# Kernel optimization log

Hardware: AMD Instinct MI355X
Metric: run time of the kernel (lower is better)

## Reference

```python
import jax, jax.numpy as jnp
import numpy as np

W_NBITS = 8
A_NBITS = 8


def _fake_quant_weight_per_channel(w, nbits):
    # symmetric per-output-channel (row) fake quantization
    qmax = float(2 ** (nbits - 1) - 1)
    scale = jnp.max(jnp.abs(w), axis=1, keepdims=True) / qmax  # [out, 1]
    scale = jnp.maximum(scale, 1e-8)
    return jnp.clip(jnp.round(w / scale), -qmax - 1.0, qmax) * scale


def _fake_quant_act_per_group(x, group_size, nbits):
    # dynamic symmetric per-group fake quantization along the feature dim
    qmax = float(2 ** (nbits - 1) - 1)
    tokens, feat = x.shape
    xg = x.reshape(tokens, feat // group_size, group_size)
    scale = jnp.max(jnp.abs(xg), axis=-1, keepdims=True) / qmax  # [T, G, 1]
    scale = jnp.maximum(scale, 1e-8)
    xq = jnp.clip(jnp.round(xg / scale), -qmax - 1.0, qmax) * scale
    return xq.reshape(tokens, feat)


def setup_inputs() -> dict:
    key = jax.random.key(0)
    k1, k2, k3 = jax.random.split(key, 3)
    tokens, in_f, out_f = 8192, 4096, 4096
    x = jax.random.normal(k1, (tokens, in_f), dtype=jnp.float32)
    weight = jax.random.normal(k2, (out_f, in_f), dtype=jnp.float32) * 0.02
    bias = jax.random.normal(k3, (out_f,), dtype=jnp.float32) * 0.02
    return {"x": x, "weight": weight, "bias": bias, "group_size": 128}


def reference(x, weight, bias, group_size):
    w_q = _fake_quant_weight_per_channel(weight, W_NBITS)
    x_q = _fake_quant_act_per_group(x, group_size, A_NBITS)
    # F.linear: x @ w.T + b
    return jnp.einsum("tc,oc->to", x_q, w_q) + bias
```

## Files before the change

kernel.cpp:

```cpp
#include <hip/hip_runtime.h>
#include <stdint.h>


typedef __attribute__((ext_vector_type(4))) int   i32x4;
typedef __attribute__((ext_vector_type(4))) float f32x4;

static __device__ __forceinline__ void load_lds16(const void* g, void* l) {
    __builtin_amdgcn_global_load_lds(
        (const __attribute__((address_space(1))) void*)g,
        (__attribute__((address_space(3))) void*)l, 16, 0, 0);
}

static __device__ __forceinline__ int8_t q8m(float v, float inv) {
    float q = rintf(v * inv);
    q = fminf(fmaxf(q, -128.0f), 127.0f);
    return (int8_t)(int)q;
}

__global__ __launch_bounds__(256) void quant_act_kernel(
        const float* __restrict__ x, int8_t* __restrict__ xq,
        float* __restrict__ sxT, int M) {
    const int row = blockIdx.x, t = threadIdx.x;
    const float* xr = x + (size_t)row * 4096;
    float4 v[4];
#pragma unroll
    for (int i = 0; i < 4; i++)
        v[i] = *(const float4*)(xr + t * 16 + i * 4);
    float m = 0.0f;
#pragma unroll
    for (int i = 0; i < 4; i++)
        m = fmaxf(m, fmaxf(fmaxf(fabsf(v[i].x), fabsf(v[i].y)),
                           fmaxf(fabsf(v[i].z), fabsf(v[i].w))));
    m = fmaxf(m, __shfl_xor(m, 1));
    m = fmaxf(m, __shfl_xor(m, 2));
    m = fmaxf(m, __shfl_xor(m, 4));
    const float scale = fmaxf(m / 127.0f, 1e-8f);
    const float inv = 1.0f / scale;
    union { int8_t b[16]; i32x4 w; } o;
#pragma unroll
    for (int i = 0; i < 4; i++) {
        o.b[i * 4 + 0] = q8m(v[i].x, inv);
        o.b[i * 4 + 1] = q8m(v[i].y, inv);
        o.b[i * 4 + 2] = q8m(v[i].z, inv);
        o.b[i * 4 + 3] = q8m(v[i].w, inv);
    }
    *(i32x4*)(xq + (size_t)row * 4096 + t * 16) = o.w;
    if ((t & 7) == 0)
        sxT[(size_t)(t >> 3) * M + row] = scale;
}

__global__ __launch_bounds__(256) void quant_wgt_kernel(
        const float* __restrict__ w, int8_t* __restrict__ wq,
        float* __restrict__ sw) {
    const int row = blockIdx.x, t = threadIdx.x;
    const float* wr = w + (size_t)row * 4096;
    float4 v[4];
#pragma unroll
    for (int i = 0; i < 4; i++)
        v[i] = *(const float4*)(wr + t * 16 + i * 4);
    float m = 0.0f;
#pragma unroll
    for (int i = 0; i < 4; i++)
        m = fmaxf(m, fmaxf(fmaxf(fabsf(v[i].x), fabsf(v[i].y)),
                           fmaxf(fabsf(v[i].z), fabsf(v[i].w))));
#pragma unroll
    for (int off = 1; off < 64; off <<= 1)
        m = fmaxf(m, __shfl_xor(m, off));
    __shared__ float wm[4];
    if ((t & 63) == 0) wm[t >> 6] = m;
    __syncthreads();
    m = fmaxf(fmaxf(wm[0], wm[1]), fmaxf(wm[2], wm[3]));
    const float scale = fmaxf(m / 127.0f, 1e-8f);
    if (t == 0) sw[row] = scale;
    const float inv = 1.0f / scale;
    union { int8_t b[16]; i32x4 w4; } o;
#pragma unroll
    for (int i = 0; i < 4; i++) {
        o.b[i * 4 + 0] = q8m(v[i].x, inv);
        o.b[i * 4 + 1] = q8m(v[i].y, inv);
        o.b[i * 4 + 2] = q8m(v[i].z, inv);
        o.b[i * 4 + 3] = q8m(v[i].w, inv);
    }
    *(i32x4*)(wq + (size_t)row * 4096 + t * 16) = o.w4;
}

#define QUAD(mh, nh)                                                         \
    _Pragma("unroll")                                                        \
    for (int mi2 = 0; mi2 < 4; ++mi2) {                                      \
        _Pragma("unroll")                                                    \
        for (int nj = 0; nj < 2; ++nj) {                                     \
            const int ni = (nh) * 2 + nj;                                    \
            i32x4 t = __builtin_amdgcn_mfma_i32_16x16x64_i8(                 \
                a[mi2][0], b[ni][0], (i32x4){0, 0, 0, 0}, 0, 0, 0);          \
            t = __builtin_amdgcn_mfma_i32_16x16x64_i8(                       \
                a[mi2][1], b[ni][1], t, 0, 0, 0);                            \
            _Pragma("unroll")                                                \
            for (int r = 0; r < 4; ++r)                                      \
                acc[(mh) * 4 + mi2][ni][r] += (float)t[r] * sxv[mi2][r];     \
        }                                                                    \
    }

__global__ __launch_bounds__(512, 2) void gemm_i8_kernel(
        const int8_t* __restrict__ A, const int8_t* __restrict__ B,
        const float* __restrict__ sxT, const float* __restrict__ sw,
        const float* __restrict__ bias, float* __restrict__ C,
        int M, int N, int K) {
    __shared__ __align__(16) int8_t As[2][256 * 128];
    __shared__ __align__(16) int8_t Bs[2][256 * 128];
    const int tid = threadIdx.x;
    const int wave = tid >> 6, lane = tid & 63;

    const int nwg = gridDim.x, nN = N >> 8;
    const int wg = ((int)blockIdx.x & 7) * (nwg >> 3) + ((int)blockIdx.x >> 3);
    const int bm = (wg / nN) << 8, bn = (wg % nN) << 8;

    const int wm = (wave >> 2) << 7, wn = (wave & 3) << 6;
    const int fr = lane & 15, q = lane >> 4, r7 = lane & 7;

    const int srow = wave * 8 + (lane >> 3);
    const int scol = ((lane & 7) ^ ((lane >> 3) & 7)) << 4;
    const size_t sK = (size_t)K;
    const int8_t* Ag = A + (size_t)(bm + srow) * sK + scol;
    const int8_t* Bg = B + (size_t)(bn + srow) * sK + scol;
    const int sldsw = wave * 8 * 128;

    f32x4 acc[8][4];
#pragma unroll
    for (int i = 0; i < 8; i++)
#pragma unroll
        for (int jn = 0; jn < 4; jn++) acc[i][jn] = (f32x4){0.f, 0.f, 0.f, 0.f};

    const int abase = (wm + fr) * 128;
    const int bbase = (wn + fr) * 128;
    const int c0 = (q ^ r7) << 4, c1 = ((4 + q) ^ r7) << 4;
    const float* sxw = sxT + bm + wm + q * 4;

    const int NT = K >> 7;

    load_lds16(Bg,             &Bs[0][sldsw]);
    load_lds16(Bg +  64 * sK,  &Bs[0][ 64 * 128 + sldsw]);
    load_lds16(Bg + 128 * sK,  &Bs[0][128 * 128 + sldsw]);
    load_lds16(Bg + 192 * sK,  &Bs[0][192 * 128 + sldsw]);
    load_lds16(Ag,             &As[0][sldsw]);
    load_lds16(Ag + 128 * sK,  &As[0][128 * 128 + sldsw]);
    load_lds16(Ag +  64 * sK,  &As[0][ 64 * 128 + sldsw]);
    load_lds16(Ag + 192 * sK,  &As[0][192 * 128 + sldsw]);
    asm volatile("s_waitcnt vmcnt(2)" ::: "memory");
    __builtin_amdgcn_s_barrier();

    for (int j = 0; j < NT; ++j) {
        const int cur = j & 1, nxt = cur ^ 1;
        const size_t kn = (size_t)((j + 1 < NT) ? j + 1 : j) << 7;
        const int8_t* Ac = As[cur];
        const int8_t* Bc = Bs[cur];
        const float* sxg = sxw + (size_t)j * M;

        i32x4 a[4][2], b[4][2];
        f32x4 sxv[4];

#pragma unroll
        for (int i = 0; i < 4; ++i) {
            a[i][0] = *(const i32x4*)(Ac + abase + i * 2048 + c0);
            a[i][1] = *(const i32x4*)(Ac + abase + i * 2048 + c1);
            b[i][0] = *(const i32x4*)(Bc + bbase + i * 2048 + c0);
            b[i][1] = *(const i32x4*)(Bc + bbase + i * 2048 + c1);
        }
#pragma unroll
        for (int i = 0; i < 4; ++i)
            sxv[i] = *(const f32x4*)(sxg + i * 16);
        load_lds16(Bg + kn,            &Bs[nxt][sldsw]);
        load_lds16(Bg + kn + 64 * sK,  &Bs[nxt][64 * 128 + sldsw]);
        __builtin_amdgcn_s_barrier();
        asm volatile("s_waitcnt lgkmcnt(0)" ::: "memory");
        __builtin_amdgcn_sched_barrier(0);
        __builtin_amdgcn_s_setprio(1);
        QUAD(0, 0)
        __builtin_amdgcn_s_setprio(0);
        __builtin_amdgcn_s_barrier();

        load_lds16(Bg + kn + 128 * sK, &Bs[nxt][128 * 128 + sldsw]);
        load_lds16(Bg + kn + 192 * sK, &Bs[nxt][192 * 128 + sldsw]);
        __builtin_amdgcn_s_barrier();
        __builtin_amdgcn_sched_barrier(0);
        __builtin_amdgcn_s_setprio(1);
        QUAD(0, 1)
        __builtin_amdgcn_s_setprio(0);
        asm volatile("s_waitcnt vmcnt(4)" ::: "memory");
        __builtin_amdgcn_s_barrier();

#pragma unroll
        for (int i = 0; i < 4; ++i) {
            a[i][0] = *(const i32x4*)(Ac + abase + 64 * 128 + i * 2048 + c0);
            a[i][1] = *(const i32x4*)(Ac + abase + 64 * 128 + i * 2048 + c1);
        }
#pragma unroll
        for (int i = 0; i < 4; ++i)
            sxv[i] = *(const f32x4*)(sxg + 64 + i * 16);
        load_lds16(Ag + kn,            &As[nxt][sldsw]);
        load_lds16(Ag + kn + 128 * sK, &As[nxt][128 * 128 + sldsw]);
        __builtin_amdgcn_s_barrier();
        asm volatile("s_waitcnt lgkmcnt(0)" ::: "memory");
        __builtin_amdgcn_sched_barrier(0);
        __builtin_amdgcn_s_setprio(1);
        QUAD(1, 0)
        __builtin_amdgcn_s_setprio(0);
        __builtin_amdgcn_s_barrier();

        load_lds16(Ag + kn + 64 * sK,  &As[nxt][64 * 128 + sldsw]);
        load_lds16(Ag + kn + 192 * sK, &As[nxt][192 * 128 + sldsw]);
        __builtin_amdgcn_s_barrier();
        __builtin_amdgcn_sched_barrier(0);
        __builtin_amdgcn_s_setprio(1);
        QUAD(1, 1)
        __builtin_amdgcn_s_setprio(0);
        asm volatile("s_waitcnt vmcnt(2)" ::: "memory");
        __builtin_amdgcn_s_barrier();
    }
    asm volatile("s_waitcnt vmcnt(0)" ::: "memory");

    const int or0 = bm + wm + q * 4;
    const int oc0 = bn + wn + fr;
    float swv[4], bv[4];
#pragma unroll
    for (int ni = 0; ni < 4; ni++) {
        swv[ni] = sw[oc0 + ni * 16];
        bv[ni] = bias[oc0 + ni * 16];
    }
#pragma unroll
    for (int mi = 0; mi < 8; mi++)
#pragma unroll
        for (int ni = 0; ni < 4; ni++)
#pragma unroll
            for (int r = 0; r < 4; r++)
                C[(size_t)(or0 + mi * 16 + r) * N + (oc0 + ni * 16)] =
                    acc[mi][ni][r] * swv[ni] + bv[ni];
}

extern "C" void kernel_launch(void* const* d_in, const int* in_sizes, int n_in,
                              void* d_out, int out_size, void* d_ws, size_t ws_size,
                              hipStream_t stream) {
    const float* x    = (const float*)d_in[0];
    const float* w    = (const float*)d_in[1];
    const float* bias = (const float*)d_in[2];

    const int out_f  = in_sizes[2];
    const int in_f   = in_sizes[1] / out_f;
    const int tokens = in_sizes[0] / in_f;
    const int G = in_f / 128;

    int8_t* xq  = (int8_t*)d_ws;
    int8_t* wq  = xq + (size_t)tokens * in_f;
    float*  sxT = (float*)(wq + (size_t)out_f * in_f);
    float*  sw  = sxT + (size_t)G * tokens;
    float*  out = (float*)d_out;

    quant_act_kernel<<<tokens, 256, 0, stream>>>(x, xq, sxT, tokens);
    quant_wgt_kernel<<<out_f, 256, 0, stream>>>(w, wq, sw);

    const int nwg = (tokens / 256) * (out_f / 256);
    gemm_i8_kernel<<<nwg, 512, 0, stream>>>(xq, wq, sxT, sw, bias, out,
                                            tokens, out_f, in_f);
}
```

Measured before the change: 475.4 us.

## Prefetch activation scales a tile ahead and reload B fragments per half-phase

Per-group activation scales for the next K tile are now fetched from global memory at the end of each iteration into an 8-entry register array, instead of being loaded synchronously right before each compute phase. This hides the scale load latency behind the LDS-to-global pipeline, and the vmcnt waits are adjusted to match. B fragments are now loaded two at a time just before each compute phase, which reduces register pressure but adds extra LDS reads and waits. MFMAs are grouped four at a time per B column to lengthen independent chains before the scale-and-accumulate step.

```diff
diff --git a/kernel.cpp b/kernel.cpp
--- a/kernel.cpp
+++ b/kernel.cpp
@@ -84,20 +84,23 @@
     *(i32x4*)(wq + (size_t)row * 4096 + t * 16) = o.w4;
 }
 
-#define QUAD(mh, nh)                                                         \
+#define COMPUTE(mh, nh)                                                      \
     _Pragma("unroll")                                                        \
-    for (int mi2 = 0; mi2 < 4; ++mi2) {                                      \
+    for (int g = 0; g < 2; ++g) {                                            \
+        i32x4 it[4];                                                         \
         _Pragma("unroll")                                                    \
-        for (int nj = 0; nj < 2; ++nj) {                                     \
-            const int ni = (nh) * 2 + nj;                                    \
-            i32x4 t = __builtin_amdgcn_mfma_i32_16x16x64_i8(                 \
-                a[mi2][0], b[ni][0], (i32x4){0, 0, 0, 0}, 0, 0, 0);          \
-            t = __builtin_amdgcn_mfma_i32_16x16x64_i8(                       \
-                a[mi2][1], b[ni][1], t, 0, 0, 0);                            \
+        for (int mi = 0; mi < 4; ++mi) {                                     \
+            it[mi] = __builtin_amdgcn_mfma_i32_16x16x64_i8(                  \
+                a[mi][0], b[g][0], (i32x4){0, 0, 0, 0}, 0, 0, 0);            \
+            it[mi] = __builtin_amdgcn_mfma_i32_16x16x64_i8(                  \
+                a[mi][1], b[g][1], it[mi], 0, 0, 0);                         \
+        }                                                                    \
+        _Pragma("unroll")                                                    \
+        for (int mi = 0; mi < 4; ++mi)                                       \
             _Pragma("unroll")                                                \
             for (int r = 0; r < 4; ++r)                                      \
-                acc[(mh) * 4 + mi2][ni][r] += (float)t[r] * sxv[mi2][r];     \
-        }                                                                    \
+                acc[(mh) * 4 + mi][(nh) * 2 + g][r] +=                       \
+                    (float)it[mi][r] * sxn[(mh) * 4 + mi][r];                \
     }
 
 __global__ __launch_bounds__(512, 2) void gemm_i8_kernel(
@@ -133,7 +136,7 @@
     const int abase = (wm + fr) * 128;
     const int bbase = (wn + fr) * 128;
     const int c0 = (q ^ r7) << 4, c1 = ((4 + q) ^ r7) << 4;
-    const float* sxw = sxT + bm + wm + q * 4;
+    const float* sxp = sxT + bm + wm + q * 4;
 
     const int NT = K >> 7;
 
@@ -145,7 +148,11 @@
     load_lds16(Ag + 128 * sK,  &As[0][128 * 128 + sldsw]);
     load_lds16(Ag +  64 * sK,  &As[0][ 64 * 128 + sldsw]);
     load_lds16(Ag + 192 * sK,  &As[0][192 * 128 + sldsw]);
-    asm volatile("s_waitcnt vmcnt(2)" ::: "memory");
+    f32x4 sxn[8];
+#pragma unroll
+    for (int i = 0; i < 8; ++i)
+        sxn[i] = *(const f32x4*)(sxp + (i >> 2) * 64 + (i & 3) * 16);
+    asm volatile("s_waitcnt vmcnt(10)" ::: "memory");
     __builtin_amdgcn_s_barrier();
 
     for (int j = 0; j < NT; ++j) {
@@ -153,37 +160,41 @@
         const size_t kn = (size_t)((j + 1 < NT) ? j + 1 : j) << 7;
         const int8_t* Ac = As[cur];
         const int8_t* Bc = Bs[cur];
-        const float* sxg = sxw + (size_t)j * M;
-
-        i32x4 a[4][2], b[4][2];
-        f32x4 sxv[4];
+
+        i32x4 a[4][2], b[2][2];
 
 #pragma unroll
         for (int i = 0; i < 4; ++i) {
             a[i][0] = *(const i32x4*)(Ac + abase + i * 2048 + c0);
             a[i][1] = *(const i32x4*)(Ac + abase + i * 2048 + c1);
+        }
+#pragma unroll
+        for (int i = 0; i < 2; ++i) {
             b[i][0] = *(const i32x4*)(Bc + bbase + i * 2048 + c0);
             b[i][1] = *(const i32x4*)(Bc + bbase + i * 2048 + c1);
         }
-#pragma unroll
-        for (int i = 0; i < 4; ++i)
-            sxv[i] = *(const f32x4*)(sxg + i * 16);
         load_lds16(Bg + kn,            &Bs[nxt][sldsw]);
         load_lds16(Bg + kn + 64 * sK,  &Bs[nxt][64 * 128 + sldsw]);
         __builtin_amdgcn_s_barrier();
         asm volatile("s_waitcnt lgkmcnt(0)" ::: "memory");
         __builtin_amdgcn_sched_barrier(0);
         __builtin_amdgcn_s_setprio(1);
-        QUAD(0, 0)
-        __builtin_amdgcn_s_setprio(0);
-        __builtin_amdgcn_s_barrier();
-
+        COMPUTE(0, 0)
+        __builtin_amdgcn_s_setprio(0);
+        __builtin_amdgcn_s_barrier();
+
+#pragma unroll
+        for (int i = 0; i < 2; ++i) {
+            b[i][0] = *(const i32x4*)(Bc + bbase + (2 + i) * 2048 + c0);
+            b[i][1] = *(const i32x4*)(Bc + bbase + (2 + i) * 2048 + c1);
+        }
         load_lds16(Bg + kn + 128 * sK, &Bs[nxt][128 * 128 + sldsw]);
         load_lds16(Bg + kn + 192 * sK, &Bs[nxt][192 * 128 + sldsw]);
         __builtin_amdgcn_s_barrier();
-        __builtin_amdgcn_sched_barrier(0);
-        __builtin_amdgcn_s_setprio(1);
-        QUAD(0, 1)
+        asm volatile("s_waitcnt lgkmcnt(0)" ::: "memory");
+        __builtin_amdgcn_sched_barrier(0);
+        __builtin_amdgcn_s_setprio(1);
+        COMPUTE(0, 1)
         __builtin_amdgcn_s_setprio(0);
         asm volatile("s_waitcnt vmcnt(4)" ::: "memory");
         __builtin_amdgcn_s_barrier();
@@ -194,26 +205,40 @@
             a[i][1] = *(const i32x4*)(Ac + abase + 64 * 128 + i * 2048 + c1);
         }
 #pragma unroll
-        for (int i = 0; i < 4; ++i)
-            sxv[i] = *(const f32x4*)(sxg + 64 + i * 16);
+        for (int i = 0; i < 2; ++i) {
+            b[i][0] = *(const i32x4*)(Bc + bbase + i * 2048 + c0);
+            b[i][1] = *(const i32x4*)(Bc + bbase + i * 2048 + c1);
+        }
         load_lds16(Ag + kn,            &As[nxt][sldsw]);
         load_lds16(Ag + kn + 128 * sK, &As[nxt][128 * 128 + sldsw]);
         __builtin_amdgcn_s_barrier();
         asm volatile("s_waitcnt lgkmcnt(0)" ::: "memory");
         __builtin_amdgcn_sched_barrier(0);
         __builtin_amdgcn_s_setprio(1);
-        QUAD(1, 0)
-        __builtin_amdgcn_s_setprio(0);
-        __builtin_amdgcn_s_barrier();
-
+        COMPUTE(1, 0)
+        __builtin_amdgcn_s_setprio(0);
+        __builtin_amdgcn_s_barrier();
+
+#pragma unroll
+        for (int i = 0; i < 2; ++i) {
+            b[i][0] = *(const i32x4*)(Bc + bbase + (2 + i) * 2048 + c0);
+            b[i][1] = *(const i32x4*)(Bc + bbase + (2 + i) * 2048 + c1);
+        }
         load_lds16(Ag + kn + 64 * sK,  &As[nxt][64 * 128 + sldsw]);
         load_lds16(Ag + kn + 192 * sK, &As[nxt][192 * 128 + sldsw]);
         __builtin_amdgcn_s_barrier();
-        __builtin_amdgcn_sched_barrier(0);
-        __builtin_amdgcn_s_setprio(1);
-        QUAD(1, 1)
-        __builtin_amdgcn_s_setprio(0);
-        asm volatile("s_waitcnt vmcnt(2)" ::: "memory");
+        asm volatile("s_waitcnt lgkmcnt(0)" ::: "memory");
+        __builtin_amdgcn_sched_barrier(0);
+        __builtin_amdgcn_s_setprio(1);
+        COMPUTE(1, 1)
+        __builtin_amdgcn_s_setprio(0);
+        {
+            const float* sxg = sxp + (size_t)((j + 1 < NT) ? j + 1 : j) * M;
+#pragma unroll
+            for (int i = 0; i < 8; ++i)
+                sxn[i] = *(const f32x4*)(sxg + (i >> 2) * 64 + (i & 3) * 16);
+        }
+        asm volatile("s_waitcnt vmcnt(10)" ::: "memory");
         __builtin_amdgcn_s_barrier();
     }
     asm volatile("s_waitcnt vmcnt(0)" ::: "memory");
```

After: 487.1 us. +2.4%, slower.
